# Kernel tuning notes

Measured on AMD Instinct MI355X. Metric: run time of the kernel, lower is better.

The kernel has to match this reference:

```python
import jax, jax.numpy as jnp
import numpy as np
from jax import lax

LUT_SIZE = 33
BACKBONE_SIZE = 256
N_BASIS = 3


def _identity_lut(size):
    coords = jnp.linspace(0.0, 1.0, size)
    r, g, b = jnp.meshgrid(coords, coords, coords, indexing='ij')
    return jnp.stack([r.ravel(), g.ravel(), b.ravel()], axis=-1)  # [size^3, 3]


def setup_inputs() -> dict:
    key = jax.random.key(0)
    k_img, k_lut, k1, k2, kd = jax.random.split(key, 5)
    B, H, W = 4, 1080, 1920
    image = jax.random.uniform(k_img, (B, 3, H, W), dtype=jnp.float32)
    ident = _identity_lut(LUT_SIZE)  # [35937, 3]
    basis_luts = ident[None].repeat(N_BASIS, axis=0) + 0.05 * jax.random.normal(k_lut, (N_BASIS, LUT_SIZE ** 3, 3), dtype=jnp.float32)
    conv1_w = jax.random.normal(k1, (16, 3, 3, 3), dtype=jnp.float32) * 0.1
    conv1_b = jnp.zeros((16,), jnp.float32)
    conv2_w = jax.random.normal(k2, (32, 16, 3, 3), dtype=jnp.float32) * 0.1
    conv2_b = jnp.zeros((32,), jnp.float32)
    dense_w = jax.random.normal(kd, (32, 3), dtype=jnp.float32) * 0.1
    dense_b = jnp.zeros((3,), jnp.float32)
    return {"image": image, "basis_luts": basis_luts, "conv1_w": conv1_w, "conv1_b": conv1_b,
            "conv2_w": conv2_w, "conv2_b": conv2_b, "dense_w": dense_w, "dense_b": dense_b}


def _backbone(thumb, conv1_w, conv1_b, conv2_w, conv2_b, dense_w, dense_b):
    # Lightweight CNN -> softmax weights over basis LUTs. [B,3,256,256] -> [B,n_basis]
    x = lax.conv_general_dilated(thumb, conv1_w, (2, 2), 'SAME') + conv1_b[None, :, None, None]
    x = jax.nn.relu(x)
    x = lax.conv_general_dilated(x, conv2_w, (2, 2), 'SAME') + conv2_b[None, :, None, None]
    x = jax.nn.relu(x)
    x = x.mean(axis=(2, 3))  # global average pool -> [B, 32]
    return jax.nn.softmax(x @ dense_w + dense_b, axis=-1)


def _apply_lut(image, lut):
    # image [B,3,H,W] in [0,1]; lut [B,S,S,S,3] laid out as (r,g,b) grid axes.
    # Replicates F.grid_sample(mode='bilinear', padding_mode='border', align_corners=True)
    # on a 5D volume where grid x-coord = R channel -> LUT's b-axis (last grid axis),
    # y = G -> g-axis, z = B -> r-axis (exactly the axis mapping of the torch code).
    B, C, H, W = image.shape
    S = lut.shape[1]
    px = image.transpose(0, 2, 3, 1).reshape(B, H * W, 3)  # [B,P,3] = (R,G,B)
    pos = jnp.clip(px, 0.0, 1.0) * (S - 1)  # align_corners=True + border clamp
    i0 = jnp.clip(jnp.floor(pos).astype(jnp.int32), 0, S - 2)
    f = pos - i0.astype(pos.dtype)
    i1 = i0 + 1
    # axis mapping: z (LUT axis 0) <- channel 2 (Blue); y (axis 1) <- G; x (axis 2) <- R
    z0, y0, x0 = i0[..., 2], i0[..., 1], i0[..., 0]
    z1, y1, x1 = i1[..., 2], i1[..., 1], i1[..., 0]
    fz, fy, fx = f[..., 2], f[..., 1], f[..., 0]
    lut_flat = lut.reshape(B, S * S * S, 3)

    def gather(z, y, x):
        idx = (z * S + y) * S + x  # [B,P]
        return jnp.take_along_axis(lut_flat, idx[..., None], axis=1)  # [B,P,3]

    wz0, wz1 = (1.0 - fz)[..., None], fz[..., None]
    wy0, wy1 = (1.0 - fy)[..., None], fy[..., None]
    wx0, wx1 = (1.0 - fx)[..., None], fx[..., None]
    out = (wz0 * (wy0 * (wx0 * gather(z0, y0, x0) + wx1 * gather(z0, y0, x1))
                  + wy1 * (wx0 * gather(z0, y1, x0) + wx1 * gather(z0, y1, x1)))
           + wz1 * (wy0 * (wx0 * gather(z1, y0, x0) + wx1 * gather(z1, y0, x1))
                    + wy1 * (wx0 * gather(z1, y1, x0) + wx1 * gather(z1, y1, x1))))
    out = out.reshape(B, H, W, 3).transpose(0, 3, 1, 2)
    return jnp.clip(out, 0.0, 1.0)


def reference(image, basis_luts, conv1_w, conv1_b, conv2_w, conv2_b, dense_w, dense_b):
    B = image.shape[0]
    S = LUT_SIZE
    thumb = jax.image.resize(image, (B, 3, BACKBONE_SIZE, BACKBONE_SIZE), method='linear')
    weights = _backbone(thumb, conv1_w, conv1_b, conv2_w, conv2_b, dense_w, dense_b)  # [B,n]
    blended = jnp.einsum('bn,npc->bpc', weights, basis_luts)  # [B, S^3, 3]
    lut = blended.reshape(B, S, S, S, 3)
    return _apply_lut(image, lut)
```

## Files before the change

kernel.cpp:

```cpp
#include <hip/hip_runtime.h>
#include <hip/hip_bf16.h>
#include <hip/hip_fp16.h>

#define LUT_S 33
#define LUT_P (LUT_S*LUT_S*LUT_S)
#define CELLS 32768
#define IMG_H 1080
#define IMG_W 1920
#define TH 256
#define TW 256

typedef float f4 __attribute__((ext_vector_type(4)));

__global__ __launch_bounds__(256)
void resize_w_kernel(const float* __restrict__ img, float* __restrict__ tmp) {
    __shared__ float srow[IMG_W];
    int r = blockIdx.x;
    const float4* row4 = (const float4*)(img + (size_t)r * IMG_W);
    float4* s4 = (float4*)srow;
    for (int i = threadIdx.x; i < IMG_W / 4; i += 256) s4[i] = row4[i];
    __syncthreads();
    int ow = threadIdx.x;
    const float kscale = 7.5f;
    float sf = (ow + 0.5f) * 7.5f - 0.5f;
    int lo = (int)ceilf(sf - kscale); if (lo < 0) lo = 0;
    int hi = (int)floorf(sf + kscale); if (hi > IMG_W - 1) hi = IMG_W - 1;
    float acc = 0.f, wsum = 0.f;
    for (int i = lo; i <= hi; ++i) {
        float w = 1.0f - fabsf(sf - (float)i) * (1.0f / 7.5f);
        if (w > 0.f) { acc += w * srow[i]; wsum += w; }
    }
    tmp[(size_t)r * TW + ow] = acc / wsum;
}

__global__ void resize_h_kernel(const float* __restrict__ tmp,
                                float* __restrict__ thumb, int total) {
    int e = blockIdx.x * blockDim.x + threadIdx.x;
    if (e >= total) return;
    int ow = e & 255;
    int oh = (e >> 8) & 255;
    int pl = e >> 16;
    const float kscale = 4.21875f;
    float sf = (oh + 0.5f) * 4.21875f - 0.5f;
    int lo = (int)ceilf(sf - kscale); if (lo < 0) lo = 0;
    int hi = (int)floorf(sf + kscale); if (hi > IMG_H - 1) hi = IMG_H - 1;
    const float* col = tmp + (size_t)pl * IMG_H * TW + ow;
    float acc = 0.f, wsum = 0.f;
    for (int i = lo; i <= hi; ++i) {
        float w = 1.0f - fabsf(sf - (float)i) * (1.0f / 4.21875f);
        if (w > 0.f) { acc += w * col[(size_t)i * TW]; wsum += w; }
    }
    thumb[e] = acc / wsum;
}

__global__ void conv1_kernel(const float* __restrict__ thumb,
                             const float* __restrict__ w,
                             const float* __restrict__ bias,
                             float* __restrict__ out, int total) {
    int e = blockIdx.x * blockDim.x + threadIdx.x;
    if (e >= total) return;
    int ow = e & 127;
    int oh = (e >> 7) & 127;
    int g  = (e >> 14) & 3;
    int b  = e >> 16;
    float acc[4];
    #pragma unroll
    for (int j = 0; j < 4; ++j) acc[j] = bias[g * 4 + j];
    for (int ic = 0; ic < 3; ++ic) {
        const float* tp = thumb + ((size_t)(b * 3 + ic) << 16);
        #pragma unroll
        for (int kh = 0; kh < 3; ++kh) {
            int ih = oh * 2 + kh;
            if (ih >= 256) continue;
            #pragma unroll
            for (int kw = 0; kw < 3; ++kw) {
                int iw = ow * 2 + kw;
                if (iw >= 256) continue;
                float v = tp[(ih << 8) + iw];
                #pragma unroll
                for (int j = 0; j < 4; ++j)
                    acc[j] += v * w[((g * 4 + j) * 3 + ic) * 9 + kh * 3 + kw];
            }
        }
    }
    size_t o = ((size_t)(b * 16 + g * 4) << 14) + (oh << 7) + ow;
    #pragma unroll
    for (int j = 0; j < 4; ++j)
        out[o + ((size_t)j << 14)] = fmaxf(acc[j], 0.f);
}

__global__ void conv2_pool_kernel(const float* __restrict__ c1,
                                  const float* __restrict__ w,
                                  const float* __restrict__ bias,
                                  float* __restrict__ partial, int total) {
    int e = blockIdx.x * blockDim.x + threadIdx.x;
    if (e >= total) return;
    int sp = e & 4095;
    int g  = (e >> 12) & 15;
    int b  = e >> 16;
    int ow = sp & 63, oh = sp >> 6;
    float acc[2];
    #pragma unroll
    for (int j = 0; j < 2; ++j) acc[j] = bias[g * 2 + j];
    for (int ic = 0; ic < 16; ++ic) {
        const float* ip = c1 + ((size_t)(b * 16 + ic) << 14);
        #pragma unroll
        for (int kh = 0; kh < 3; ++kh) {
            int ih = oh * 2 + kh;
            if (ih >= 128) continue;
            #pragma unroll
            for (int kw = 0; kw < 3; ++kw) {
                int iw = ow * 2 + kw;
                if (iw >= 128) continue;
                float v = ip[(ih << 7) + iw];
                #pragma unroll
                for (int j = 0; j < 2; ++j)
                    acc[j] += v * w[((g * 2 + j) * 16 + ic) * 9 + kh * 3 + kw];
            }
        }
    }
    #pragma unroll
    for (int j = 0; j < 2; ++j) {
        float val = fmaxf(acc[j], 0.f);
        #pragma unroll
        for (int off = 32; off > 0; off >>= 1) val += __shfl_down(val, off, 64);
        acc[j] = val;
    }
    if ((threadIdx.x & 63) == 0) {
        #pragma unroll
        for (int j = 0; j < 2; ++j)
            partial[((b * 32 + g * 2 + j) << 6) + oh] = acc[j];
    }
}

__global__ void head_kernel(const float* __restrict__ partial,
                            const float* __restrict__ dw,
                            const float* __restrict__ db,
                            float* __restrict__ wts, int B) {
    __shared__ float sp[8 * 32];
    __shared__ float lg[8 * 3];
    int t = threadIdx.x;
    if (t < B * 32) {
        const float4* p4 = (const float4*)(partial + (t << 6));
        float s = 0.f;
        #pragma unroll
        for (int i = 0; i < 16; ++i) {
            float4 v = p4[i];
            s += v.x + v.y + v.z + v.w;
        }
        sp[t] = s * (1.0f / 4096.0f);
    }
    __syncthreads();
    if (t < B * 3) {
        int b = t / 3, n = t - b * 3;
        float acc = db[n];
        for (int ch = 0; ch < 32; ++ch) acc += sp[b * 32 + ch] * dw[ch * 3 + n];
        lg[t] = acc;
    }
    __syncthreads();
    if (t < B) {
        float a = lg[t * 3 + 0], bb = lg[t * 3 + 1], c = lg[t * 3 + 2];
        float m = fmaxf(a, fmaxf(bb, c));
        float e0 = expf(a - m), e1 = expf(bb - m), e2 = expf(c - m);
        float inv = 1.0f / (e0 + e1 + e2);
        wts[t * 3 + 0] = e0 * inv;
        wts[t * 3 + 1] = e1 * inv;
        wts[t * 3 + 2] = e2 * inv;
    }
}

__global__ void blend_cells_kernel(const float* __restrict__ basis,
                                   const float* __restrict__ wts,
                                   uint4* __restrict__ cells, int total) {
    int e = blockIdx.x * blockDim.x + threadIdx.x;
    if (e >= total) return;
    int b    = e >> 15;
    int cidx = e & (CELLS - 1);
    int cx = cidx & 31, cy = (cidx >> 5) & 31, cz = cidx >> 10;
    float w0 = wts[b * 3 + 0], w1 = wts[b * 3 + 1], w2 = wts[b * 3 + 2];
    const float* b0 = basis;
    const float* b1 = basis + (size_t)LUT_P * 3;
    const float* b2 = basis + (size_t)2 * LUT_P * 3;
    float v[24];
    float mn = 1e30f, mx = -1e30f;
    #pragma unroll
    for (int c = 0; c < 8; ++c) {
        int dx = c & 1, dy = (c >> 1) & 1, dz = c >> 2;
        size_t o = (size_t)(((cz + dz) * LUT_S + cy + dy) * LUT_S + cx + dx) * 3;
        #pragma unroll
        for (int ch = 0; ch < 3; ++ch) {
            float val = w0 * b0[o + ch] + w1 * b1[o + ch] + w2 * b2[o + ch];
            v[ch * 8 + c] = val;
            mn = fminf(mn, val); mx = fmaxf(mx, val);
        }
    }
    float range = mx - mn;
    float inv = (range > 1e-20f) ? 255.0f / range : 0.0f;
    float scale = range * (1.0f / 255.0f);
    unsigned int d[6];
    #pragma unroll
    for (int k = 0; k < 6; ++k) {
        unsigned int pk = 0;
        #pragma unroll
        for (int j = 0; j < 4; ++j) {
            float q = (v[k * 4 + j] - mn) * inv;
            int qi = (int)rintf(q);
            qi = qi < 0 ? 0 : (qi > 255 ? 255 : qi);
            pk |= ((unsigned int)qi) << (8 * j);
        }
        d[k] = pk;
    }
    uint4* outp = cells + ((size_t)e << 1);
    outp[0] = make_uint4(d[0], d[1], d[2], d[3]);
    outp[1] = make_uint4(d[4], d[5], __float_as_uint(scale), __float_as_uint(mn));
}

__device__ __forceinline__ float trilerp_u8(unsigned int lo, unsigned int hi,
                                            float fx, float fy, float fz) {
    float q000 = (float)(lo & 0xffu);
    float q100 = (float)((lo >> 8) & 0xffu);
    float q010 = (float)((lo >> 16) & 0xffu);
    float q110 = (float)((lo >> 24) & 0xffu);
    float q001 = (float)(hi & 0xffu);
    float q101 = (float)((hi >> 8) & 0xffu);
    float q011 = (float)((hi >> 16) & 0xffu);
    float q111 = (float)((hi >> 24) & 0xffu);
    float a0 = q000 + fx * (q100 - q000);
    float a1 = q010 + fx * (q110 - q010);
    float b0 = q001 + fx * (q101 - q001);
    float b1 = q011 + fx * (q111 - q011);
    float c0 = a0 + fy * (a1 - a0);
    float c1 = b0 + fy * (b1 - b0);
    return c0 + fz * (c1 - c0);
}

__global__ __launch_bounds__(256)
void apply_lut_kernel(const float* __restrict__ img,
                      const uint4* __restrict__ cells,
                      float* __restrict__ out, int total_quads) {
    const int P  = IMG_H * IMG_W;
    const int QP = P / 4;
    int t = blockIdx.x * blockDim.x + threadIdx.x;
    if (t >= total_quads) return;
    int b = t / QP;
    int q = t - b * QP;
    const uint4* cbase = cells + ((size_t)b * CELLS << 1);
    size_t base = (size_t)b * 3 * P + (size_t)q * 4;
    f4 R  = *(const f4*)(img + base);
    f4 G  = *(const f4*)(img + base + P);
    f4 Bl = *(const f4*)(img + base + 2 * (size_t)P);

    int cidx[4]; float fx[4], fy[4], fz[4];
    #pragma unroll
    for (int k = 0; k < 4; ++k) {
        float pr = fminf(fmaxf(R[k], 0.f), 1.f) * (float)(LUT_S - 1);
        float pg = fminf(fmaxf(G[k], 0.f), 1.f) * (float)(LUT_S - 1);
        float pb = fminf(fmaxf(Bl[k], 0.f), 1.f) * (float)(LUT_S - 1);
        int ix = (int)pr; if (ix > LUT_S - 2) ix = LUT_S - 2;
        int iy = (int)pg; if (iy > LUT_S - 2) iy = LUT_S - 2;
        int iz = (int)pb; if (iz > LUT_S - 2) iz = LUT_S - 2;
        fx[k] = pr - (float)ix;
        fy[k] = pg - (float)iy;
        fz[k] = pb - (float)iz;
        cidx[k] = (iz << 10) | (iy << 5) | ix;
    }
    uint4 A[4], Bq[4];
    #pragma unroll
    for (int k = 0; k < 4; ++k) {
        const uint4* cp = cbase + ((size_t)cidx[k] << 1);
        A[k]  = cp[0];
        Bq[k] = cp[1];
    }
    f4 Ro, Go, Bo;
    #pragma unroll
    for (int k = 0; k < 4; ++k) {
        float scale = __uint_as_float(Bq[k].z);
        float offs  = __uint_as_float(Bq[k].w);
        float tr = trilerp_u8(A[k].x, A[k].y, fx[k], fy[k], fz[k]);
        float tg = trilerp_u8(A[k].z, A[k].w, fx[k], fy[k], fz[k]);
        float tb = trilerp_u8(Bq[k].x, Bq[k].y, fx[k], fy[k], fz[k]);
        Ro[k] = fminf(fmaxf(tr * scale + offs, 0.f), 1.f);
        Go[k] = fminf(fmaxf(tg * scale + offs, 0.f), 1.f);
        Bo[k] = fminf(fmaxf(tb * scale + offs, 0.f), 1.f);
    }
    __builtin_nontemporal_store(Ro, (f4*)(out + base));
    __builtin_nontemporal_store(Go, (f4*)(out + base + P));
    __builtin_nontemporal_store(Bo, (f4*)(out + base + 2 * (size_t)P));
}

extern "C" void kernel_launch(void* const* d_in, const int* in_sizes, int n_in,
                              void* d_out, int out_size, void* d_ws, size_t ws_size,
                              hipStream_t stream) {
    const float* img     = (const float*)d_in[0];
    const float* basis   = (const float*)d_in[1];
    const float* conv1_w = (const float*)d_in[2];
    const float* conv1_b = (const float*)d_in[3];
    const float* conv2_w = (const float*)d_in[4];
    const float* conv2_b = (const float*)d_in[5];
    const float* dense_w = (const float*)d_in[6];
    const float* dense_b = (const float*)d_in[7];
    float* out = (float*)d_out;

    const size_t P = (size_t)IMG_H * IMG_W;
    int B = (int)(in_sizes[0] / (3 * P));

    float* ws = (float*)d_ws;
    size_t off = 0;
    float* tmp1    = ws + off; off += (size_t)B * 3 * IMG_H * TW;
    float* thumb   = ws + off; off += (size_t)B * 3 * TH * TW;
    float* c1      = ws + off; off += (size_t)B * 16 * 128 * 128;
    float* partial = ws + off; off += (size_t)B * 32 * 64;
    float* wts     = ws + off; off += (size_t)B * 3;
    off = (off + 3) & ~(size_t)3;
    uint4* cells   = (uint4*)(ws + off); off += (size_t)B * CELLS * 8;

    const int TPB = 256;
    {
        resize_w_kernel<<<B * 3 * IMG_H, TPB, 0, stream>>>(img, tmp1);
    }
    {
        int total = B * 3 * TH * TW;
        resize_h_kernel<<<(total + TPB - 1) / TPB, TPB, 0, stream>>>(tmp1, thumb, total);
    }
    {
        int total = B * 4 * 128 * 128;
        conv1_kernel<<<(total + TPB - 1) / TPB, TPB, 0, stream>>>(thumb, conv1_w, conv1_b, c1, total);
    }
    {
        int total = B * 16 * 4096;
        conv2_pool_kernel<<<(total + TPB - 1) / TPB, TPB, 0, stream>>>(c1, conv2_w, conv2_b, partial, total);
    }
    {
        head_kernel<<<1, TPB, 0, stream>>>(partial, dense_w, dense_b, wts, B);
    }
    {
        int total = B * CELLS;
        blend_cells_kernel<<<(total + TPB - 1) / TPB, TPB, 0, stream>>>(basis, wts, cells, total);
    }
    {
        int total = B * (int)(P / 4);
        apply_lut_kernel<<<(total + TPB - 1) / TPB, TPB, 0, stream>>>(img, cells, out, total);
    }
}
```

Baseline: 289.2 us.

## Fuse backbone stages into one persistent cooperative kernel with grid syncs

Replaces the six backbone kernels (resize W, resize H, conv1, conv2+pool, head, blend/quantize) with one persistent cooperative kernel of 512 blocks that steps through phases separated by grid-wide syncs. The head softmax is folded into the blend phase, with every block recomputing the weights in shared memory, so the separate weights buffer is gone. The aim is to remove kernel launch gaps and tail effects between the small stages. In exchange, each phase uses grid-stride loops over a fixed block count, so the large resize phase may get less parallelism, and a per-phase launch fallback is kept in case the cooperative launch fails.

```diff
diff --git a/kernel.cpp b/kernel.cpp
--- a/kernel.cpp
+++ b/kernel.cpp
@@ -1,6 +1,7 @@
 #include <hip/hip_runtime.h>
-#include <hip/hip_bf16.h>
-#include <hip/hip_fp16.h>
+#include <hip/hip_cooperative_groups.h>
+
+namespace cg = cooperative_groups;
 
 #define LUT_S 33
 #define LUT_P (LUT_S*LUT_S*LUT_S)
@@ -9,210 +10,227 @@
 #define IMG_W 1920
 #define TH 256
 #define TW 256
+#define NBLK 512
+#define TPB 256
 
 typedef float f4 __attribute__((ext_vector_type(4)));
 
-__global__ __launch_bounds__(256)
-void resize_w_kernel(const float* __restrict__ img, float* __restrict__ tmp) {
+__global__ __launch_bounds__(TPB, 2)
+void backbone_mega(const float* __restrict__ img,
+                   const float* __restrict__ basis,
+                   const float* __restrict__ c1w, const float* __restrict__ c1b,
+                   const float* __restrict__ c2w, const float* __restrict__ c2b,
+                   const float* __restrict__ dw,  const float* __restrict__ db,
+                   float* __restrict__ tmp1, float* __restrict__ thumb,
+                   float* __restrict__ c1,   float* __restrict__ partial,
+                   uint4* __restrict__ cells, int B,
+                   int phase_lo, int phase_hi)
+{
+    const int tid = threadIdx.x;
+    const int bid = blockIdx.x;
+    const int nblk = gridDim.x;
+
     __shared__ float srow[IMG_W];
-    int r = blockIdx.x;
-    const float4* row4 = (const float4*)(img + (size_t)r * IMG_W);
-    float4* s4 = (float4*)srow;
-    for (int i = threadIdx.x; i < IMG_W / 4; i += 256) s4[i] = row4[i];
-    __syncthreads();
-    int ow = threadIdx.x;
-    const float kscale = 7.5f;
-    float sf = (ow + 0.5f) * 7.5f - 0.5f;
-    int lo = (int)ceilf(sf - kscale); if (lo < 0) lo = 0;
-    int hi = (int)floorf(sf + kscale); if (hi > IMG_W - 1) hi = IMG_W - 1;
-    float acc = 0.f, wsum = 0.f;
-    for (int i = lo; i <= hi; ++i) {
-        float w = 1.0f - fabsf(sf - (float)i) * (1.0f / 7.5f);
-        if (w > 0.f) { acc += w * srow[i]; wsum += w; }
-    }
-    tmp[(size_t)r * TW + ow] = acc / wsum;
-}
-
-__global__ void resize_h_kernel(const float* __restrict__ tmp,
-                                float* __restrict__ thumb, int total) {
-    int e = blockIdx.x * blockDim.x + threadIdx.x;
-    if (e >= total) return;
-    int ow = e & 255;
-    int oh = (e >> 8) & 255;
-    int pl = e >> 16;
-    const float kscale = 4.21875f;
-    float sf = (oh + 0.5f) * 4.21875f - 0.5f;
-    int lo = (int)ceilf(sf - kscale); if (lo < 0) lo = 0;
-    int hi = (int)floorf(sf + kscale); if (hi > IMG_H - 1) hi = IMG_H - 1;
-    const float* col = tmp + (size_t)pl * IMG_H * TW + ow;
-    float acc = 0.f, wsum = 0.f;
-    for (int i = lo; i <= hi; ++i) {
-        float w = 1.0f - fabsf(sf - (float)i) * (1.0f / 4.21875f);
-        if (w > 0.f) { acc += w * col[(size_t)i * TW]; wsum += w; }
-    }
-    thumb[e] = acc / wsum;
-}
-
-__global__ void conv1_kernel(const float* __restrict__ thumb,
-                             const float* __restrict__ w,
-                             const float* __restrict__ bias,
-                             float* __restrict__ out, int total) {
-    int e = blockIdx.x * blockDim.x + threadIdx.x;
-    if (e >= total) return;
-    int ow = e & 127;
-    int oh = (e >> 7) & 127;
-    int g  = (e >> 14) & 3;
-    int b  = e >> 16;
-    float acc[4];
-    #pragma unroll
-    for (int j = 0; j < 4; ++j) acc[j] = bias[g * 4 + j];
-    for (int ic = 0; ic < 3; ++ic) {
-        const float* tp = thumb + ((size_t)(b * 3 + ic) << 16);
-        #pragma unroll
-        for (int kh = 0; kh < 3; ++kh) {
-            int ih = oh * 2 + kh;
-            if (ih >= 256) continue;
-            #pragma unroll
-            for (int kw = 0; kw < 3; ++kw) {
-                int iw = ow * 2 + kw;
-                if (iw >= 256) continue;
-                float v = tp[(ih << 8) + iw];
+    __shared__ float sh_sp[256];
+    __shared__ float sh_w[32];
+
+    for (int ph = phase_lo; ph <= phase_hi; ++ph) {
+        if (ph != phase_lo) {
+            cg::this_grid().sync();
+        }
+        switch (ph) {
+
+        case 0: {
+            int nrows = B * 3 * IMG_H;
+            for (int r = bid; r < nrows; r += nblk) {
+                const float4* row4 = (const float4*)(img + (size_t)r * IMG_W);
+                float4* s4 = (float4*)srow;
+                for (int i = tid; i < IMG_W / 4; i += TPB) s4[i] = row4[i];
+                __syncthreads();
+                int ow = tid;
+                float sf = (ow + 0.5f) * 7.5f - 0.5f;
+                int lo = (int)ceilf(sf - 7.5f); if (lo < 0) lo = 0;
+                int hi = (int)floorf(sf + 7.5f); if (hi > IMG_W - 1) hi = IMG_W - 1;
+                float acc = 0.f, wsum = 0.f;
+                for (int i = lo; i <= hi; ++i) {
+                    float w = 1.0f - fabsf(sf - (float)i) * (1.0f / 7.5f);
+                    if (w > 0.f) { acc += w * srow[i]; wsum += w; }
+                }
+                tmp1[(size_t)r * TW + ow] = acc / wsum;
+                __syncthreads();
+            }
+        } break;
+
+        case 1: {
+            int total = B * 3 * TH * TW;
+            for (int e = bid * TPB + tid; e < total; e += nblk * TPB) {
+                int ow = e & 255;
+                int oh = (e >> 8) & 255;
+                int pl = e >> 16;
+                float sf = (oh + 0.5f) * 4.21875f - 0.5f;
+                int lo = (int)ceilf(sf - 4.21875f); if (lo < 0) lo = 0;
+                int hi = (int)floorf(sf + 4.21875f); if (hi > IMG_H - 1) hi = IMG_H - 1;
+                const float* col = tmp1 + (size_t)pl * IMG_H * TW + ow;
+                float acc = 0.f, wsum = 0.f;
+                for (int i = lo; i <= hi; ++i) {
+                    float w = 1.0f - fabsf(sf - (float)i) * (1.0f / 4.21875f);
+                    if (w > 0.f) { acc += w * col[(size_t)i * TW]; wsum += w; }
+                }
+                thumb[e] = acc / wsum;
+            }
+        } break;
+
+        case 2: {
+            int total = B * 4 * 128 * 128;
+            for (int e = bid * TPB + tid; e < total; e += nblk * TPB) {
+                int ow = e & 127;
+                int oh = (e >> 7) & 127;
+                int g  = (e >> 14) & 3;
+                int b  = e >> 16;
+                float acc[4];
+                #pragma unroll
+                for (int j = 0; j < 4; ++j) acc[j] = c1b[g * 4 + j];
+                for (int ic = 0; ic < 3; ++ic) {
+                    const float* tp = thumb + ((size_t)(b * 3 + ic) << 16);
+                    #pragma unroll
+                    for (int kh = 0; kh < 3; ++kh) {
+                        int ih = oh * 2 + kh;
+                        if (ih >= 256) continue;
+                        #pragma unroll
+                        for (int kw = 0; kw < 3; ++kw) {
+                            int iw = ow * 2 + kw;
+                            if (iw >= 256) continue;
+                            float v = tp[(ih << 8) + iw];
+                            #pragma unroll
+                            for (int j = 0; j < 4; ++j)
+                                acc[j] += v * c1w[((g * 4 + j) * 3 + ic) * 9 + kh * 3 + kw];
+                        }
+                    }
+                }
+                size_t o = ((size_t)(b * 16 + g * 4) << 14) + (oh << 7) + ow;
                 #pragma unroll
                 for (int j = 0; j < 4; ++j)
-                    acc[j] += v * w[((g * 4 + j) * 3 + ic) * 9 + kh * 3 + kw];
-            }
+                    c1[o + ((size_t)j << 14)] = fmaxf(acc[j], 0.f);
+            }
+        } break;
+
+        case 3: {
+            int total = B * 16 * 4096;
+            for (int e = bid * TPB + tid; e < total; e += nblk * TPB) {
+                int sp = e & 4095;
+                int g  = (e >> 12) & 15;
+                int b  = e >> 16;
+                int ow = sp & 63, oh = sp >> 6;
+                float acc[2];
+                #pragma unroll
+                for (int j = 0; j < 2; ++j) acc[j] = c2b[g * 2 + j];
+                for (int ic = 0; ic < 16; ++ic) {
+                    const float* ip = c1 + ((size_t)(b * 16 + ic) << 14);
+                    #pragma unroll
+                    for (int kh = 0; kh < 3; ++kh) {
+                        int ih = oh * 2 + kh;
+                        if (ih >= 128) continue;
+                        #pragma unroll
+                        for (int kw = 0; kw < 3; ++kw) {
+                            int iw = ow * 2 + kw;
+                            if (iw >= 128) continue;
+                            float v = ip[(ih << 7) + iw];
+                            #pragma unroll
+                            for (int j = 0; j < 2; ++j)
+                                acc[j] += v * c2w[((g * 2 + j) * 16 + ic) * 9 + kh * 3 + kw];
+                        }
+                    }
+                }
+                #pragma unroll
+                for (int j = 0; j < 2; ++j) {
+                    float val = fmaxf(acc[j], 0.f);
+                    #pragma unroll
+                    for (int off = 32; off > 0; off >>= 1) val += __shfl_down(val, off, 64);
+                    acc[j] = val;
+                }
+                if ((tid & 63) == 0) {
+                    #pragma unroll
+                    for (int j = 0; j < 2; ++j)
+                        partial[((b * 32 + g * 2 + j) << 6) + oh] = acc[j];
+                }
+            }
+        } break;
+
+        case 4: {
+            if (tid < B * 32) {
+                const float4* p4 = (const float4*)(partial + (tid << 6));
+                float s = 0.f;
+                #pragma unroll
+                for (int i = 0; i < 16; ++i) {
+                    float4 v = p4[i];
+                    s += v.x + v.y + v.z + v.w;
+                }
+                sh_sp[tid] = s * (1.0f / 4096.0f);
+            }
+            __syncthreads();
+            if (tid < B * 3) {
+                int b = tid / 3, n = tid - b * 3;
+                float acc = db[n];
+                for (int ch = 0; ch < 32; ++ch) acc += sh_sp[b * 32 + ch] * dw[ch * 3 + n];
+                sh_w[tid] = acc;
+            }
+            __syncthreads();
+            if (tid < B) {
+                float a = sh_w[tid * 3 + 0], bb = sh_w[tid * 3 + 1], c = sh_w[tid * 3 + 2];
+                float m = fmaxf(a, fmaxf(bb, c));
+                float e0 = expf(a - m), e1 = expf(bb - m), e2 = expf(c - m);
+                float inv = 1.0f / (e0 + e1 + e2);
+                sh_w[tid * 3 + 0] = e0 * inv;
+                sh_w[tid * 3 + 1] = e1 * inv;
+                sh_w[tid * 3 + 2] = e2 * inv;
+            }
+            __syncthreads();
+
+            int total = B * CELLS;
+            for (int e = bid * TPB + tid; e < total; e += nblk * TPB) {
+                int b    = e >> 15;
+                int cidx = e & (CELLS - 1);
+                int cx = cidx & 31, cy = (cidx >> 5) & 31, cz = cidx >> 10;
+                float w0 = sh_w[b * 3 + 0], w1 = sh_w[b * 3 + 1], w2 = sh_w[b * 3 + 2];
+                const float* b0 = basis;
+                const float* b1 = basis + (size_t)LUT_P * 3;
+                const float* b2 = basis + (size_t)2 * LUT_P * 3;
+                float v[24];
+                float mn = 1e30f, mx = -1e30f;
+                #pragma unroll
+                for (int c = 0; c < 8; ++c) {
+                    int dx = c & 1, dy = (c >> 1) & 1, dz = c >> 2;
+                    size_t o = (size_t)(((cz + dz) * LUT_S + cy + dy) * LUT_S + cx + dx) * 3;
+                    #pragma unroll
+                    for (int ch = 0; ch < 3; ++ch) {
+                        float val = w0 * b0[o + ch] + w1 * b1[o + ch] + w2 * b2[o + ch];
+                        v[ch * 8 + c] = val;
+                        mn = fminf(mn, val); mx = fmaxf(mx, val);
+                    }
+                }
+                float range = mx - mn;
+                float inv = (range > 1e-20f) ? 255.0f / range : 0.0f;
+                float scale = range * (1.0f / 255.0f);
+                unsigned int d[6];
+                #pragma unroll
+                for (int k = 0; k < 6; ++k) {
+                    unsigned int pk = 0;
+                    #pragma unroll
+                    for (int j = 0; j < 4; ++j) {
+                        float q = (v[k * 4 + j] - mn) * inv;
+                        int qi = (int)rintf(q);
+                        qi = qi < 0 ? 0 : (qi > 255 ? 255 : qi);
+                        pk |= ((unsigned int)qi) << (8 * j);
+                    }
+                    d[k] = pk;
+                }
+                uint4* outp = cells + ((size_t)e << 1);
+                outp[0] = make_uint4(d[0], d[1], d[2], d[3]);
+                outp[1] = make_uint4(d[4], d[5], __float_as_uint(scale), __float_as_uint(mn));
+            }
+        } break;
         }
     }
-    size_t o = ((size_t)(b * 16 + g * 4) << 14) + (oh << 7) + ow;
-    #pragma unroll
-    for (int j = 0; j < 4; ++j)
-        out[o + ((size_t)j << 14)] = fmaxf(acc[j], 0.f);
-}
-
-__global__ void conv2_pool_kernel(const float* __restrict__ c1,
-                                  const float* __restrict__ w,
-                                  const float* __restrict__ bias,
-                                  float* __restrict__ partial, int total) {
-    int e = blockIdx.x * blockDim.x + threadIdx.x;
-    if (e >= total) return;
-    int sp = e & 4095;
-    int g  = (e >> 12) & 15;
-    int b  = e >> 16;
-    int ow = sp & 63, oh = sp >> 6;
-    float acc[2];
-    #pragma unroll
-    for (int j = 0; j < 2; ++j) acc[j] = bias[g * 2 + j];
-    for (int ic = 0; ic < 16; ++ic) {
-        const float* ip = c1 + ((size_t)(b * 16 + ic) << 14);
-        #pragma unroll
-        for (int kh = 0; kh < 3; ++kh) {
-            int ih = oh * 2 + kh;
-            if (ih >= 128) continue;
-            #pragma unroll
-            for (int kw = 0; kw < 3; ++kw) {
-                int iw = ow * 2 + kw;
-                if (iw >= 128) continue;
-                float v = ip[(ih << 7) + iw];
-                #pragma unroll
-                for (int j = 0; j < 2; ++j)
-                    acc[j] += v * w[((g * 2 + j) * 16 + ic) * 9 + kh * 3 + kw];
-            }
-        }
-    }
-    #pragma unroll
-    for (int j = 0; j < 2; ++j) {
-        float val = fmaxf(acc[j], 0.f);
-        #pragma unroll
-        for (int off = 32; off > 0; off >>= 1) val += __shfl_down(val, off, 64);
-        acc[j] = val;
-    }
-    if ((threadIdx.x & 63) == 0) {
-        #pragma unroll
-        for (int j = 0; j < 2; ++j)
-            partial[((b * 32 + g * 2 + j) << 6) + oh] = acc[j];
-    }
-}
-
-__global__ void head_kernel(const float* __restrict__ partial,
-                            const float* __restrict__ dw,
-                            const float* __restrict__ db,
-                            float* __restrict__ wts, int B) {
-    __shared__ float sp[8 * 32];
-    __shared__ float lg[8 * 3];
-    int t = threadIdx.x;
-    if (t < B * 32) {
-        const float4* p4 = (const float4*)(partial + (t << 6));
-        float s = 0.f;
-        #pragma unroll
-        for (int i = 0; i < 16; ++i) {
-            float4 v = p4[i];
-            s += v.x + v.y + v.z + v.w;
-        }
-        sp[t] = s * (1.0f / 4096.0f);
-    }
-    __syncthreads();
-    if (t < B * 3) {
-        int b = t / 3, n = t - b * 3;
-        float acc = db[n];
-        for (int ch = 0; ch < 32; ++ch) acc += sp[b * 32 + ch] * dw[ch * 3 + n];
-        lg[t] = acc;
-    }
-    __syncthreads();
-    if (t < B) {
-        float a = lg[t * 3 + 0], bb = lg[t * 3 + 1], c = lg[t * 3 + 2];
-        float m = fmaxf(a, fmaxf(bb, c));
-        float e0 = expf(a - m), e1 = expf(bb - m), e2 = expf(c - m);
-        float inv = 1.0f / (e0 + e1 + e2);
-        wts[t * 3 + 0] = e0 * inv;
-        wts[t * 3 + 1] = e1 * inv;
-        wts[t * 3 + 2] = e2 * inv;
-    }
-}
-
-__global__ void blend_cells_kernel(const float* __restrict__ basis,
-                                   const float* __restrict__ wts,
-                                   uint4* __restrict__ cells, int total) {
-    int e = blockIdx.x * blockDim.x + threadIdx.x;
-    if (e >= total) return;
-    int b    = e >> 15;
-    int cidx = e & (CELLS - 1);
-    int cx = cidx & 31, cy = (cidx >> 5) & 31, cz = cidx >> 10;
-    float w0 = wts[b * 3 + 0], w1 = wts[b * 3 + 1], w2 = wts[b * 3 + 2];
-    const float* b0 = basis;
-    const float* b1 = basis + (size_t)LUT_P * 3;
-    const float* b2 = basis + (size_t)2 * LUT_P * 3;
-    float v[24];
-    float mn = 1e30f, mx = -1e30f;
-    #pragma unroll
-    for (int c = 0; c < 8; ++c) {
-        int dx = c & 1, dy = (c >> 1) & 1, dz = c >> 2;
-        size_t o = (size_t)(((cz + dz) * LUT_S + cy + dy) * LUT_S + cx + dx) * 3;
-        #pragma unroll
-        for (int ch = 0; ch < 3; ++ch) {
-            float val = w0 * b0[o + ch] + w1 * b1[o + ch] + w2 * b2[o + ch];
-            v[ch * 8 + c] = val;
-            mn = fminf(mn, val); mx = fmaxf(mx, val);
-        }
-    }
-    float range = mx - mn;
-    float inv = (range > 1e-20f) ? 255.0f / range : 0.0f;
-    float scale = range * (1.0f / 255.0f);
-    unsigned int d[6];
-    #pragma unroll
-    for (int k = 0; k < 6; ++k) {
-        unsigned int pk = 0;
-        #pragma unroll
-        for (int j = 0; j < 4; ++j) {
-            float q = (v[k * 4 + j] - mn) * inv;
-            int qi = (int)rintf(q);
-            qi = qi < 0 ? 0 : (qi > 255 ? 255 : qi);
-            pk |= ((unsigned int)qi) << (8 * j);
-        }
-        d[k] = pk;
-    }
-    uint4* outp = cells + ((size_t)e << 1);
-    outp[0] = make_uint4(d[0], d[1], d[2], d[3]);
-    outp[1] = make_uint4(d[4], d[5], __float_as_uint(scale), __float_as_uint(mn));
 }
 
 __device__ __forceinline__ float trilerp_u8(unsigned int lo, unsigned int hi,
@@ -310,35 +328,33 @@
     float* thumb   = ws + off; off += (size_t)B * 3 * TH * TW;
     float* c1      = ws + off; off += (size_t)B * 16 * 128 * 128;
     float* partial = ws + off; off += (size_t)B * 32 * 64;
-    float* wts     = ws + off; off += (size_t)B * 3;
     off = (off + 3) & ~(size_t)3;
     uint4* cells   = (uint4*)(ws + off); off += (size_t)B * CELLS * 8;
 
-    const int TPB = 256;
     {
-        resize_w_kernel<<<B * 3 * IMG_H, TPB, 0, stream>>>(img, tmp1);
-    }
-    {
-        int total = B * 3 * TH * TW;
-        resize_h_kernel<<<(total + TPB - 1) / TPB, TPB, 0, stream>>>(tmp1, thumb, total);
-    }
-    {
-        int total = B * 4 * 128 * 128;
-        conv1_kernel<<<(total + TPB - 1) / TPB, TPB, 0, stream>>>(thumb, conv1_w, conv1_b, c1, total);
-    }
-    {
-        int total = B * 16 * 4096;
-        conv2_pool_kernel<<<(total + TPB - 1) / TPB, TPB, 0, stream>>>(c1, conv2_w, conv2_b, partial, total);
-    }
-    {
-        head_kernel<<<1, TPB, 0, stream>>>(partial, dense_w, dense_b, wts, B);
-    }
-    {
-        int total = B * CELLS;
-        blend_cells_kernel<<<(total + TPB - 1) / TPB, TPB, 0, stream>>>(basis, wts, cells, total);
+        int p_lo = 0, p_hi = 4;
+        void* kargs[] = {
+            (void*)&img, (void*)&basis,
+            (void*)&conv1_w, (void*)&conv1_b,
+            (void*)&conv2_w, (void*)&conv2_b,
+            (void*)&dense_w, (void*)&dense_b,
+            (void*)&tmp1, (void*)&thumb, (void*)&c1, (void*)&partial,
+            (void*)&cells, (void*)&B, (void*)&p_lo, (void*)&p_hi
+        };
+        hipError_t cerr = hipLaunchCooperativeKernel(backbone_mega, dim3(NBLK), dim3(TPB),
+                                                     kargs, 0, stream);
+        if (cerr != hipSuccess) {
+            (void)hipGetLastError();
+            for (int ph = 0; ph < 5; ++ph) {
+                backbone_mega<<<NBLK, TPB, 0, stream>>>(
+                    img, basis, conv1_w, conv1_b, conv2_w, conv2_b,
+                    dense_w, dense_b, tmp1, thumb, c1, partial,
+                    cells, B, ph, ph);
+            }
+        }
     }
     {
         int total = B * (int)(P / 4);
-        apply_lut_kernel<<<(total + TPB - 1) / TPB, TPB, 0, stream>>>(img, cells, out, total);
+        apply_lut_kernel<<<(total + 255) / 256, 256, 0, stream>>>(img, cells, out, total);
     }
 }
```

Result: slower. 591.6 us (+104.5%).
